# Kernel optimization log

Hardware: AMD Instinct MI355X
Metric: run time of the kernel (lower is better)

The kernel has to match this reference:

```python
import jax, jax.numpy as jnp
import numpy as np

B, S, DIM = 32, 1, 2048
N_HEADS, N_KV = 32, 8
HEAD_DIM = DIM // N_HEADS  # 64
MAXB, MAXS = 32, 2048
START_POS = 2047
THETA = 10000.0  # precompute_freqs_cis called without theta -> llama default


def setup_inputs() -> dict:
    key = jax.random.key(0)
    ks = jax.random.split(key, 7)
    u = lambda k, s: jax.random.uniform(k, s, jnp.float32) * 0.02  # scaled torch.rand init
    return {
        "x": jax.random.normal(ks[0], (B, S, DIM), jnp.float32),
        "q_w": u(ks[1], (DIM, N_HEADS * HEAD_DIM)),
        "k_w": u(ks[2], (DIM, N_KV * HEAD_DIM)),
        "v_w": u(ks[3], (DIM, N_KV * HEAD_DIM)),
        "o_w": u(ks[4], (DIM, N_HEADS * HEAD_DIM)),
        "cache_k": jax.random.normal(ks[5], (MAXB, MAXS, N_KV, HEAD_DIM), jnp.float32) * 0.02,
        "cache_v": jax.random.normal(ks[6], (MAXB, MAXS, N_KV, HEAD_DIM), jnp.float32) * 0.02,
        "start_pos": START_POS,
    }


def _rope(x, cos, sin):
    # x: [B, S, H, D]; consecutive pairs (even, odd) form complex numbers (llama view_as_complex)
    xr, xi = x[..., 0::2], x[..., 1::2]
    out = jnp.stack([xr * cos - xi * sin, xr * sin + xi * cos], axis=-1)
    return out.reshape(x.shape)


def _attn_fwd(x, q_w, k_w, v_w, o_w, cache_k, cache_v, start_pos):
    B_, S_, _ = x.shape
    # fused_linear(x, W) == x @ W
    xq = (x @ q_w).reshape(B_, S_, N_HEADS, HEAD_DIM)
    xk = (x @ k_w).reshape(B_, S_, N_KV, HEAD_DIM)
    xv = (x @ v_w).reshape(B_, S_, N_KV, HEAD_DIM)

    # RoPE freqs for positions [start_pos, start_pos + S)
    inv = 1.0 / (THETA ** (jnp.arange(0, HEAD_DIM, 2, dtype=jnp.float32) / HEAD_DIM))
    t = jnp.arange(start_pos, start_pos + S_, dtype=jnp.float32)
    ang = t[:, None] * inv[None, :]                    # [S, D/2]
    cos = jnp.cos(ang)[None, :, None, :]               # [1, S, 1, D/2]
    sin = jnp.sin(ang)[None, :, None, :]
    xq = _rope(xq, cos, sin)
    xk = _rope(xk, cos, sin)

    # KV-cache append
    cache_k = jax.lax.dynamic_update_slice(cache_k, xk, (0, start_pos, 0, 0))
    cache_v = jax.lax.dynamic_update_slice(cache_v, xv, (0, start_pos, 0, 0))
    L = start_pos + S_
    keys = cache_k[:B_, :L].transpose(0, 2, 1, 3)      # [B, Hkv, L, D]
    vals = cache_v[:B_, :L].transpose(0, 2, 1, 3)

    # GQA attention; grouped einsum = repeat_kv without materializing copies
    rep = N_HEADS // N_KV
    q = xq.transpose(0, 2, 1, 3).reshape(B_, N_KV, rep, S_, HEAD_DIM)
    scores = jnp.einsum('bkrsd,bkld->bkrsl', q, keys) * (HEAD_DIM ** -0.5)
    p = jax.nn.softmax(scores, axis=-1)
    o = jnp.einsum('bkrsl,bkld->bkrsd', p, vals)
    o = o.reshape(B_, N_HEADS, S_, HEAD_DIM).transpose(0, 2, 1, 3).reshape(B_, S_, -1)
    return o @ o_w


def reference(x, q_w, k_w, v_w, o_w, cache_k, cache_v, start_pos):
    return _attn_fwd(x, q_w, k_w, v_w, o_w, cache_k, cache_v, start_pos)
```

## Files before the change

### kernel.cpp

```cpp
#include <hip/hip_runtime.h>
#include <hip/hip_bf16.h>
#include <math.h>

#define NQKV 3072
#define NS 16
#define SPL 128
#define KT 128

__device__ __forceinline__ int read_sp(const int* spp) {
  if (!spp) return 2047;
  int raw = spp[0];
  if (raw >= 0 && raw < 2048) return raw;
  union { int i; float f; } u; u.i = raw;
  if (u.f >= 0.f && u.f < 2048.f) return (int)u.f;
  return 2047;
}

__global__ __launch_bounds__(256) void k_prep(const float* __restrict__ x,
                                              float* __restrict__ xt,
                                              float* __restrict__ rope,
                                              const int* __restrict__ spp) {
  int idx = blockIdx.x * 256 + threadIdx.x;
  int r = idx >> 11, k = idx & 2047;
  xt[k * 32 + r] = x[idx];
  if (blockIdx.x == 0 && threadIdx.x < 32) {
    int i = threadIdx.x;
    int sp = read_sp(spp);
    double freq = pow(10000.0, -(double)(2 * i) / 64.0);
    double ang = (double)sp * freq;
    double sd, cd; sincos(ang, &sd, &cd);
    rope[2 * i]     = (float)cd;
    rope[2 * i + 1] = (float)sd;
  }
}

__global__ __launch_bounds__(256) void k_qkv3(const float* __restrict__ qw,
                                              const float* __restrict__ kw,
                                              const float* __restrict__ vw,
                                              const float* __restrict__ xt,
                                              float* __restrict__ part, int kc) {
  int colb = blockIdx.x, j = blockIdx.y, t = threadIdx.x;
  const float* w; int ldw, col, outcol;
  if (colb < 4)       { w = qw; ldw = 2048; col = colb * 512 + t * 2; outcol = col; }
  else if (colb == 4) { w = kw; ldw = 512;  col = t * 2; outcol = 2048 + col; }
  else                { w = vw; ldw = 512;  col = t * 2; outcol = 2560 + col; }
  __shared__ __align__(16) float xs[KT][32];
  int k0 = j * kc;
  float2 acc[32];
  #pragma unroll
  for (int r = 0; r < 32; r++) { acc[r].x = 0.f; acc[r].y = 0.f; }
  for (int kt = 0; kt < kc; kt += KT) {
    int ksz = (kc - kt < KT) ? (kc - kt) : KT;
    __syncthreads();
    for (int idx = t; idx < ksz * 32; idx += 256)
      ((float*)xs)[idx] = xt[(size_t)(k0 + kt) * 32 + idx];
    __syncthreads();
    const float* wp = w + (size_t)(k0 + kt) * ldw + col;
    #pragma unroll 2
    for (int kk = 0; kk < ksz; kk++) {
      float2 wv = *(const float2*)&wp[(size_t)kk * ldw];
      #pragma unroll
      for (int r4 = 0; r4 < 8; r4++) {
        float4 xr = *(const float4*)&xs[kk][r4 * 4];
        acc[r4*4+0].x = fmaf(xr.x, wv.x, acc[r4*4+0].x);
        acc[r4*4+0].y = fmaf(xr.x, wv.y, acc[r4*4+0].y);
        acc[r4*4+1].x = fmaf(xr.y, wv.x, acc[r4*4+1].x);
        acc[r4*4+1].y = fmaf(xr.y, wv.y, acc[r4*4+1].y);
        acc[r4*4+2].x = fmaf(xr.z, wv.x, acc[r4*4+2].x);
        acc[r4*4+2].y = fmaf(xr.z, wv.y, acc[r4*4+2].y);
        acc[r4*4+3].x = fmaf(xr.w, wv.x, acc[r4*4+3].x);
        acc[r4*4+3].y = fmaf(xr.w, wv.y, acc[r4*4+3].y);
      }
    }
  }
  float* po = part + (size_t)j * (32 * NQKV) + outcol;
  #pragma unroll
  for (int r = 0; r < 32; r++) *(float2*)&po[(size_t)r * NQKV] = acc[r];
}

__global__ __launch_bounds__(256) void k_qred(const float* __restrict__ part,
                                              float* __restrict__ qred, int js) {
  int col = blockIdx.x * 256 + threadIdx.x;
  int b = blockIdx.y;
  float s = 0.f;
  for (int j = 0; j < js; j++) s += part[(size_t)j * (32 * NQKV) + (size_t)b * NQKV + col];
  qred[(size_t)b * NQKV + col] = s;
}

__global__ __launch_bounds__(512) void k_attn3(const float* __restrict__ ck,
                                               const float* __restrict__ cv,
                                               const float* __restrict__ qred,
                                               const float* __restrict__ rope,
                                               float* __restrict__ osplit,
                                               float* __restrict__ msl,
                                               const int* __restrict__ spp) {
  int s = blockIdx.x, b = blockIdx.y, tid = threadIdx.x;
  int sp = read_sp(spp);

  __shared__ __align__(16) float qs[8][4][64];
  __shared__ __align__(16) float knew[8][64];
  __shared__ __align__(16) float vnew[8][64];
  __shared__ __align__(16) float sc[8][4][SPL + 4];
  __shared__ __align__(16) float opart[4][8][4][64];

  const float* qb = qred + (size_t)b * NQKV;

  {
    int pi = tid * 2;
    #pragma unroll
    for (int u = 0; u < 2; u++, pi++) {
      int hq = pi >> 5, i = pi & 31;
      float cs = rope[2 * i], sn = rope[2 * i + 1];
      float a = qb[hq * 64 + 2 * i], bb = qb[hq * 64 + 2 * i + 1];
      qs[hq >> 2][hq & 3][2 * i]     = (a * cs - bb * sn) * 0.125f;
      qs[hq >> 2][hq & 3][2 * i + 1] = (a * sn + bb * cs) * 0.125f;
    }
    if (tid < 256) {
      int h = tid >> 5, i = tid & 31;
      float cs = rope[2 * i], sn = rope[2 * i + 1];
      float a = qb[2048 + h * 64 + 2 * i], bb = qb[2048 + h * 64 + 2 * i + 1];
      knew[h][2 * i]     = a * cs - bb * sn;
      knew[h][2 * i + 1] = a * sn + bb * cs;
    }
    { int h = tid >> 6, d = tid & 63; vnew[h][d] = qb[2560 + h * 64 + d]; }
  }
  __syncthreads();

  int w = tid >> 6, lane = tid & 63;
  int w2 = w >> 1, half = w & 1;
  int hh2 = lane >> 4, d4 = lane & 15;
  int h = half * 4 + hh2;

  float4 qv0 = *(const float4*)&qs[h][0][d4 * 4];
  float4 qv1 = *(const float4*)&qs[h][1][d4 * 4];
  float4 qv2 = *(const float4*)&qs[h][2][d4 * 4];
  float4 qv3 = *(const float4*)&qs[h][3][d4 * 4];
  float4 kn4 = *(const float4*)&knew[h][d4 * 4];
  float4 vn4 = *(const float4*)&vnew[h][d4 * 4];

  const float* kb = ck + (size_t)b * 2048 * 512 + half * 256 + lane * 4;
  int pbase = s * SPL + w2;
  #pragma unroll 4
  for (int i = 0; i < 32; i++) {
    int p = pbase + i * 4;
    float4 k4 = *(const float4*)(kb + (size_t)p * 512);
    if (p == sp) k4 = kn4;
    float s0 = qv0.x * k4.x + qv0.y * k4.y + qv0.z * k4.z + qv0.w * k4.w;
    float s1 = qv1.x * k4.x + qv1.y * k4.y + qv1.z * k4.z + qv1.w * k4.w;
    float s2 = qv2.x * k4.x + qv2.y * k4.y + qv2.z * k4.z + qv2.w * k4.w;
    float s3 = qv3.x * k4.x + qv3.y * k4.y + qv3.z * k4.z + qv3.w * k4.w;
    #pragma unroll
    for (int off = 1; off <= 8; off <<= 1) {
      s0 += __shfl_xor(s0, off);
      s1 += __shfl_xor(s1, off);
      s2 += __shfl_xor(s2, off);
      s3 += __shfl_xor(s3, off);
    }
    float sv = (d4 == 0) ? s0 : (d4 == 1) ? s1 : (d4 == 2) ? s2 : s3;
    if (d4 < 4) sc[h][d4][p - s * SPL] = sv;
  }
  __syncthreads();

  #pragma unroll
  for (int q = 0; q < 4; q++) {
    int row = w * 4 + q, rh = row >> 2, rr = row & 3;
    float2 v01 = *(const float2*)&sc[rh][rr][lane * 2];
    float m = fmaxf(v01.x, v01.y);
    #pragma unroll
    for (int off = 1; off <= 32; off <<= 1) m = fmaxf(m, __shfl_xor(m, off));
    float e0 = __expf(v01.x - m), e1 = __expf(v01.y - m);
    sc[rh][rr][lane * 2] = e0; sc[rh][rr][lane * 2 + 1] = e1;
    float l = e0 + e1;
    #pragma unroll
    for (int off = 1; off <= 32; off <<= 1) l += __shfl_xor(l, off);
    if (lane == 0) {
      size_t mi = (((size_t)b * NS + s) * 32 + row) * 2;
      msl[mi] = m; msl[mi + 1] = l;
    }
  }
  __syncthreads();

  const float* vb = cv + (size_t)b * 2048 * 512 + half * 256 + lane * 4;
  float4 a0 = {0,0,0,0}, a1 = {0,0,0,0}, a2 = {0,0,0,0}, a3 = {0,0,0,0};
  #pragma unroll 4
  for (int i = 0; i < 32; i++) {
    int p = pbase + i * 4;
    float4 v4 = *(const float4*)(vb + (size_t)p * 512);
    if (p == sp) v4 = vn4;
    int pl = p - s * SPL;
    float e0 = sc[h][0][pl], e1 = sc[h][1][pl], e2 = sc[h][2][pl], e3 = sc[h][3][pl];
    a0.x = fmaf(e0, v4.x, a0.x); a0.y = fmaf(e0, v4.y, a0.y);
    a0.z = fmaf(e0, v4.z, a0.z); a0.w = fmaf(e0, v4.w, a0.w);
    a1.x = fmaf(e1, v4.x, a1.x); a1.y = fmaf(e1, v4.y, a1.y);
    a1.z = fmaf(e1, v4.z, a1.z); a1.w = fmaf(e1, v4.w, a1.w);
    a2.x = fmaf(e2, v4.x, a2.x); a2.y = fmaf(e2, v4.y, a2.y);
    a2.z = fmaf(e2, v4.z, a2.z); a2.w = fmaf(e2, v4.w, a2.w);
    a3.x = fmaf(e3, v4.x, a3.x); a3.y = fmaf(e3, v4.y, a3.y);
    a3.z = fmaf(e3, v4.z, a3.z); a3.w = fmaf(e3, v4.w, a3.w);
  }
  *(float4*)&opart[w2][h][0][d4 * 4] = a0;
  *(float4*)&opart[w2][h][1][d4 * 4] = a1;
  *(float4*)&opart[w2][h][2][d4 * 4] = a2;
  *(float4*)&opart[w2][h][3][d4 * 4] = a3;
  __syncthreads();

  for (int e = tid; e < 2048; e += 512) {
    int eh = e >> 8, er = (e >> 6) & 3, ed = e & 63;
    float o = opart[0][eh][er][ed] + opart[1][eh][er][ed] +
              opart[2][eh][er][ed] + opart[3][eh][er][ed];
    osplit[(((size_t)b * NS + s) * 32 + eh * 4 + er) * 64 + ed] = o;
  }
}

__global__ __launch_bounds__(256) void k_combine3(const float* __restrict__ osplit,
                                                  const float* __restrict__ msl,
                                                  float* __restrict__ obt) {
  int b = blockIdx.x, g = blockIdx.y, t = threadIdx.x;
  int hq = g * 8 + (t >> 5);
  int d0 = (t & 31) * 2;
  float ms[NS], ls[NS];
  float m = -1e30f;
  #pragma unroll
  for (int s = 0; s < NS; s++) {
    size_t mi = (((size_t)b * NS + s) * 32 + hq) * 2;
    ms[s] = msl[mi]; ls[s] = msl[mi + 1];
    m = fmaxf(m, ms[s]);
  }
  float L = 0.f, o0 = 0.f, o1 = 0.f;
  #pragma unroll
  for (int s = 0; s < NS; s++) {
    float wgt = __expf(ms[s] - m);
    L = fmaf(wgt, ls[s], L);
    const float* op = osplit + (((size_t)b * NS + s) * 32 + hq) * 64 + d0;
    o0 = fmaf(wgt, op[0], o0);
    o1 = fmaf(wgt, op[1], o1);
  }
  float invL = 1.f / L;
  obt[(size_t)(hq * 64 + d0) * 32 + b]     = o0 * invL;
  obt[(size_t)(hq * 64 + d0 + 1) * 32 + b] = o1 * invL;
}

__global__ __launch_bounds__(256) void k_oproj3(const float* __restrict__ ow,
                                                const float* __restrict__ obt,
                                                float* __restrict__ part, int kc) {
  int colb = blockIdx.x, j = blockIdx.y, t = threadIdx.x;
  int col = colb * 512 + t * 2;
  __shared__ __align__(16) float xs[KT][32];
  int k0 = j * kc;
  float2 acc[32];
  #pragma unroll
  for (int r = 0; r < 32; r++) { acc[r].x = 0.f; acc[r].y = 0.f; }
  for (int kt = 0; kt < kc; kt += KT) {
    int ksz = (kc - kt < KT) ? (kc - kt) : KT;
    __syncthreads();
    for (int idx = t; idx < ksz * 32; idx += 256)
      ((float*)xs)[idx] = obt[(size_t)(k0 + kt) * 32 + idx];
    __syncthreads();
    const float* wp = ow + (size_t)(k0 + kt) * 2048 + col;
    #pragma unroll 2
    for (int kk = 0; kk < ksz; kk++) {
      float2 wv = *(const float2*)&wp[(size_t)kk * 2048];
      #pragma unroll
      for (int r4 = 0; r4 < 8; r4++) {
        float4 xr = *(const float4*)&xs[kk][r4 * 4];
        acc[r4*4+0].x = fmaf(xr.x, wv.x, acc[r4*4+0].x);
        acc[r4*4+0].y = fmaf(xr.x, wv.y, acc[r4*4+0].y);
        acc[r4*4+1].x = fmaf(xr.y, wv.x, acc[r4*4+1].x);
        acc[r4*4+1].y = fmaf(xr.y, wv.y, acc[r4*4+1].y);
        acc[r4*4+2].x = fmaf(xr.z, wv.x, acc[r4*4+2].x);
        acc[r4*4+2].y = fmaf(xr.z, wv.y, acc[r4*4+2].y);
        acc[r4*4+3].x = fmaf(xr.w, wv.x, acc[r4*4+3].x);
        acc[r4*4+3].y = fmaf(xr.w, wv.y, acc[r4*4+3].y);
      }
    }
  }
  float* po = part + (size_t)j * 65536 + col;
  #pragma unroll
  for (int r = 0; r < 32; r++) *(float2*)&po[(size_t)r * 2048] = acc[r];
}

__global__ __launch_bounds__(256) void k_finish(const float* __restrict__ part,
                                                float* __restrict__ out, int js) {
  int idx = blockIdx.x * 256 + threadIdx.x;
  float s = 0.f;
  for (int j = 0; j < js; j++) s += part[(size_t)j * 65536 + idx];
  out[idx] = s;
}

extern "C" void kernel_launch(void* const* d_in, const int* in_sizes, int n_in,
                              void* d_out, int out_size, void* d_ws, size_t ws_size,
                              hipStream_t stream) {
  const float* x  = (const float*)d_in[0];
  const float* qw = (const float*)d_in[1];
  const float* kw = (const float*)d_in[2];
  const float* vw = (const float*)d_in[3];
  const float* ow = (const float*)d_in[4];
  const float* ck = (const float*)d_in[5];
  const float* cv = (const float*)d_in[6];
  const int*   sp = (n_in >= 8) ? (const int*)d_in[7] : nullptr;

  const size_t FIXED = 65536 + 65536 + 98304 + 1048576 + 32768 + 64;
  int js = 2;
  {
    const int cands[5] = {32, 16, 8, 4, 2};
    for (int i = 0; i < 5; i++) {
      if ((FIXED + (size_t)cands[i] * 98304) * 4 <= ws_size) { js = cands[i]; break; }
    }
  }
  int kc = 2048 / js;

  float* ws     = (float*)d_ws;
  float* xt     = ws;
  float* part   = xt + 65536;
  float* obt    = part + (size_t)js * 98304;
  float* qred   = obt + 65536;
  float* osplit = qred + 98304;
  float* msl    = osplit + 1048576;
  float* rope   = msl + 32768;

  k_prep    <<<256,             256, 0, stream>>>(x, xt, rope, sp);
  k_qkv3    <<<dim3(6, js),     256, 0, stream>>>(qw, kw, vw, xt, part, kc);
  k_qred    <<<dim3(12, 32),    256, 0, stream>>>(part, qred, js);
  k_attn3   <<<dim3(NS, 32),    512, 0, stream>>>(ck, cv, qred, rope, osplit, msl, sp);
  k_combine3<<<dim3(32, 4),     256, 0, stream>>>(osplit, msl, obt);
  k_oproj3  <<<dim3(4, js),     256, 0, stream>>>(ow, obt, part, kc);
  k_finish  <<<256,             256, 0, stream>>>(part, (float*)d_out, js);
}
```

Baseline: 418.1 us.

## Fuse split-K reductions via atomics and use single-pass online-softmax attention

The QKV and output projections now accumulate split-K partials with atomicAdd into buffers zeroed in the prep kernel, which removes the separate reduce and finish kernels. The attention kernel switches to a single streaming pass with online softmax, reading K and V together instead of staging scores in shared memory, and each wave now covers 64 contiguous positions. Partial outputs are stored in fp16 across 32 splits per batch, and the combine step merges them. This trades two kernel launches and extra buffer traffic for atomic contention, nondeterministic summation order, and reduced precision in the intermediate attention outputs.

```diff
diff --git a/kernel.cpp b/kernel.cpp
--- a/kernel.cpp
+++ b/kernel.cpp
@@ -1,11 +1,13 @@
 #include <hip/hip_runtime.h>
+#include <hip/hip_fp16.h>
 #include <hip/hip_bf16.h>
 #include <math.h>
 
 #define NQKV 3072
-#define NS 16
-#define SPL 128
-#define KT 128
+#define NS   8
+#define SPL  256
+#define PW   64
+#define NS4  32
 
 __device__ __forceinline__ int read_sp(const int* spp) {
   if (!spp) return 2047;
@@ -16,13 +18,17 @@
   return 2047;
 }
 
-__global__ __launch_bounds__(256) void k_prep(const float* __restrict__ x,
-                                              float* __restrict__ xt,
-                                              float* __restrict__ rope,
-                                              const int* __restrict__ spp) {
+__global__ __launch_bounds__(256) void k_prep5(const float* __restrict__ x,
+                                               float* __restrict__ xt,
+                                               float* __restrict__ qkvacc,
+                                               float* __restrict__ out,
+                                               float* __restrict__ rope,
+                                               const int* __restrict__ spp) {
   int idx = blockIdx.x * 256 + threadIdx.x;
   int r = idx >> 11, k = idx & 2047;
   xt[k * 32 + r] = x[idx];
+  out[idx] = 0.f;
+  for (int z = idx; z < 32 * NQKV; z += 65536) qkvacc[z] = 0.f;
   if (blockIdx.x == 0 && threadIdx.x < 32) {
     int i = threadIdx.x;
     int sp = read_sp(spp);
@@ -34,76 +40,63 @@
   }
 }
 
-__global__ __launch_bounds__(256) void k_qkv3(const float* __restrict__ qw,
+__global__ __launch_bounds__(256) void k_qkv5(const float* __restrict__ qw,
                                               const float* __restrict__ kw,
                                               const float* __restrict__ vw,
                                               const float* __restrict__ xt,
-                                              float* __restrict__ part, int kc) {
+                                              float* __restrict__ qkvacc) {
   int colb = blockIdx.x, j = blockIdx.y, t = threadIdx.x;
   const float* w; int ldw, col, outcol;
   if (colb < 4)       { w = qw; ldw = 2048; col = colb * 512 + t * 2; outcol = col; }
   else if (colb == 4) { w = kw; ldw = 512;  col = t * 2; outcol = 2048 + col; }
   else                { w = vw; ldw = 512;  col = t * 2; outcol = 2560 + col; }
-  __shared__ __align__(16) float xs[KT][32];
-  int k0 = j * kc;
+  __shared__ __align__(16) float xs[64][32];
+  int k0 = j * 64;
+  for (int i2 = t; i2 < 64 * 32; i2 += 256)
+    ((float*)xs)[i2] = xt[(size_t)k0 * 32 + i2];
+  __syncthreads();
   float2 acc[32];
   #pragma unroll
   for (int r = 0; r < 32; r++) { acc[r].x = 0.f; acc[r].y = 0.f; }
-  for (int kt = 0; kt < kc; kt += KT) {
-    int ksz = (kc - kt < KT) ? (kc - kt) : KT;
-    __syncthreads();
-    for (int idx = t; idx < ksz * 32; idx += 256)
-      ((float*)xs)[idx] = xt[(size_t)(k0 + kt) * 32 + idx];
-    __syncthreads();
-    const float* wp = w + (size_t)(k0 + kt) * ldw + col;
-    #pragma unroll 2
-    for (int kk = 0; kk < ksz; kk++) {
-      float2 wv = *(const float2*)&wp[(size_t)kk * ldw];
-      #pragma unroll
-      for (int r4 = 0; r4 < 8; r4++) {
-        float4 xr = *(const float4*)&xs[kk][r4 * 4];
-        acc[r4*4+0].x = fmaf(xr.x, wv.x, acc[r4*4+0].x);
-        acc[r4*4+0].y = fmaf(xr.x, wv.y, acc[r4*4+0].y);
-        acc[r4*4+1].x = fmaf(xr.y, wv.x, acc[r4*4+1].x);
-        acc[r4*4+1].y = fmaf(xr.y, wv.y, acc[r4*4+1].y);
-        acc[r4*4+2].x = fmaf(xr.z, wv.x, acc[r4*4+2].x);
-        acc[r4*4+2].y = fmaf(xr.z, wv.y, acc[r4*4+2].y);
-        acc[r4*4+3].x = fmaf(xr.w, wv.x, acc[r4*4+3].x);
-        acc[r4*4+3].y = fmaf(xr.w, wv.y, acc[r4*4+3].y);
-      }
-    }
-  }
-  float* po = part + (size_t)j * (32 * NQKV) + outcol;
-  #pragma unroll
-  for (int r = 0; r < 32; r++) *(float2*)&po[(size_t)r * NQKV] = acc[r];
-}
-
-__global__ __launch_bounds__(256) void k_qred(const float* __restrict__ part,
-                                              float* __restrict__ qred, int js) {
-  int col = blockIdx.x * 256 + threadIdx.x;
-  int b = blockIdx.y;
-  float s = 0.f;
-  for (int j = 0; j < js; j++) s += part[(size_t)j * (32 * NQKV) + (size_t)b * NQKV + col];
-  qred[(size_t)b * NQKV + col] = s;
-}
-
-__global__ __launch_bounds__(512) void k_attn3(const float* __restrict__ ck,
-                                               const float* __restrict__ cv,
-                                               const float* __restrict__ qred,
-                                               const float* __restrict__ rope,
-                                               float* __restrict__ osplit,
-                                               float* __restrict__ msl,
-                                               const int* __restrict__ spp) {
+  const float* wp = w + (size_t)k0 * ldw + col;
+  #pragma unroll 4
+  for (int kk = 0; kk < 64; kk++) {
+    float2 wv = *(const float2*)&wp[(size_t)kk * ldw];
+    #pragma unroll
+    for (int r4 = 0; r4 < 8; r4++) {
+      float4 xr = *(const float4*)&xs[kk][r4 * 4];
+      acc[r4*4+0].x = fmaf(xr.x, wv.x, acc[r4*4+0].x);
+      acc[r4*4+0].y = fmaf(xr.x, wv.y, acc[r4*4+0].y);
+      acc[r4*4+1].x = fmaf(xr.y, wv.x, acc[r4*4+1].x);
+      acc[r4*4+1].y = fmaf(xr.y, wv.y, acc[r4*4+1].y);
+      acc[r4*4+2].x = fmaf(xr.z, wv.x, acc[r4*4+2].x);
+      acc[r4*4+2].y = fmaf(xr.z, wv.y, acc[r4*4+2].y);
+      acc[r4*4+3].x = fmaf(xr.w, wv.x, acc[r4*4+3].x);
+      acc[r4*4+3].y = fmaf(xr.w, wv.y, acc[r4*4+3].y);
+    }
+  }
+  #pragma unroll
+  for (int r = 0; r < 32; r++) {
+    atomicAdd(&qkvacc[(size_t)r * NQKV + outcol],     acc[r].x);
+    atomicAdd(&qkvacc[(size_t)r * NQKV + outcol + 1], acc[r].y);
+  }
+}
+
+__global__ __launch_bounds__(512, 4) void k_attn5(const float* __restrict__ ck,
+                                                  const float* __restrict__ cv,
+                                                  const float* __restrict__ qkvacc,
+                                                  const float* __restrict__ rope,
+                                                  __half* __restrict__ osplit,
+                                                  float* __restrict__ msl,
+                                                  const int* __restrict__ spp) {
   int s = blockIdx.x, b = blockIdx.y, tid = threadIdx.x;
   int sp = read_sp(spp);
 
   __shared__ __align__(16) float qs[8][4][64];
   __shared__ __align__(16) float knew[8][64];
   __shared__ __align__(16) float vnew[8][64];
-  __shared__ __align__(16) float sc[8][4][SPL + 4];
-  __shared__ __align__(16) float opart[4][8][4][64];
-
-  const float* qb = qred + (size_t)b * NQKV;
+
+  const float* qb = qkvacc + (size_t)b * NQKV;
 
   {
     int pi = tid * 2;
@@ -139,12 +132,19 @@
   float4 vn4 = *(const float4*)&vnew[h][d4 * 4];
 
   const float* kb = ck + (size_t)b * 2048 * 512 + half * 256 + lane * 4;
-  int pbase = s * SPL + w2;
+  const float* vb = cv + (size_t)b * 2048 * 512 + half * 256 + lane * 4;
+  int p0 = s * SPL + w2 * PW;
+
+  float m0 = -1e30f, m1 = -1e30f, m2 = -1e30f, m3 = -1e30f;
+  float l0 = 0.f, l1 = 0.f, l2 = 0.f, l3 = 0.f;
+  float4 o0 = {0,0,0,0}, o1 = {0,0,0,0}, o2 = {0,0,0,0}, o3 = {0,0,0,0};
+
   #pragma unroll 4
-  for (int i = 0; i < 32; i++) {
-    int p = pbase + i * 4;
+  for (int i = 0; i < PW; i++) {
+    int p = p0 + i;
     float4 k4 = *(const float4*)(kb + (size_t)p * 512);
-    if (p == sp) k4 = kn4;
+    float4 v4 = *(const float4*)(vb + (size_t)p * 512);
+    if (p == sp) { k4 = kn4; v4 = vn4; }
     float s0 = qv0.x * k4.x + qv0.y * k4.y + qv0.z * k4.z + qv0.w * k4.w;
     float s1 = qv1.x * k4.x + qv1.y * k4.y + qv1.z * k4.z + qv1.w * k4.w;
     float s2 = qv2.x * k4.x + qv2.y * k4.y + qv2.z * k4.z + qv2.w * k4.w;
@@ -156,135 +156,107 @@
       s2 += __shfl_xor(s2, off);
       s3 += __shfl_xor(s3, off);
     }
-    float sv = (d4 == 0) ? s0 : (d4 == 1) ? s1 : (d4 == 2) ? s2 : s3;
-    if (d4 < 4) sc[h][d4][p - s * SPL] = sv;
-  }
-  __syncthreads();
-
-  #pragma unroll
-  for (int q = 0; q < 4; q++) {
-    int row = w * 4 + q, rh = row >> 2, rr = row & 3;
-    float2 v01 = *(const float2*)&sc[rh][rr][lane * 2];
-    float m = fmaxf(v01.x, v01.y);
-    #pragma unroll
-    for (int off = 1; off <= 32; off <<= 1) m = fmaxf(m, __shfl_xor(m, off));
-    float e0 = __expf(v01.x - m), e1 = __expf(v01.y - m);
-    sc[rh][rr][lane * 2] = e0; sc[rh][rr][lane * 2 + 1] = e1;
-    float l = e0 + e1;
-    #pragma unroll
-    for (int off = 1; off <= 32; off <<= 1) l += __shfl_xor(l, off);
-    if (lane == 0) {
-      size_t mi = (((size_t)b * NS + s) * 32 + row) * 2;
-      msl[mi] = m; msl[mi + 1] = l;
-    }
-  }
-  __syncthreads();
-
-  const float* vb = cv + (size_t)b * 2048 * 512 + half * 256 + lane * 4;
-  float4 a0 = {0,0,0,0}, a1 = {0,0,0,0}, a2 = {0,0,0,0}, a3 = {0,0,0,0};
-  #pragma unroll 4
-  for (int i = 0; i < 32; i++) {
-    int p = pbase + i * 4;
-    float4 v4 = *(const float4*)(vb + (size_t)p * 512);
-    if (p == sp) v4 = vn4;
-    int pl = p - s * SPL;
-    float e0 = sc[h][0][pl], e1 = sc[h][1][pl], e2 = sc[h][2][pl], e3 = sc[h][3][pl];
-    a0.x = fmaf(e0, v4.x, a0.x); a0.y = fmaf(e0, v4.y, a0.y);
-    a0.z = fmaf(e0, v4.z, a0.z); a0.w = fmaf(e0, v4.w, a0.w);
-    a1.x = fmaf(e1, v4.x, a1.x); a1.y = fmaf(e1, v4.y, a1.y);
-    a1.z = fmaf(e1, v4.z, a1.z); a1.w = fmaf(e1, v4.w, a1.w);
-    a2.x = fmaf(e2, v4.x, a2.x); a2.y = fmaf(e2, v4.y, a2.y);
-    a2.z = fmaf(e2, v4.z, a2.z); a2.w = fmaf(e2, v4.w, a2.w);
-    a3.x = fmaf(e3, v4.x, a3.x); a3.y = fmaf(e3, v4.y, a3.y);
-    a3.z = fmaf(e3, v4.z, a3.z); a3.w = fmaf(e3, v4.w, a3.w);
-  }
-  *(float4*)&opart[w2][h][0][d4 * 4] = a0;
-  *(float4*)&opart[w2][h][1][d4 * 4] = a1;
-  *(float4*)&opart[w2][h][2][d4 * 4] = a2;
-  *(float4*)&opart[w2][h][3][d4 * 4] = a3;
-  __syncthreads();
-
-  for (int e = tid; e < 2048; e += 512) {
-    int eh = e >> 8, er = (e >> 6) & 3, ed = e & 63;
-    float o = opart[0][eh][er][ed] + opart[1][eh][er][ed] +
-              opart[2][eh][er][ed] + opart[3][eh][er][ed];
-    osplit[(((size_t)b * NS + s) * 32 + eh * 4 + er) * 64 + ed] = o;
-  }
-}
-
-__global__ __launch_bounds__(256) void k_combine3(const float* __restrict__ osplit,
+    float mn0 = fmaxf(m0, s0), c0 = __expf(m0 - mn0), e0 = __expf(s0 - mn0);
+    float mn1 = fmaxf(m1, s1), c1 = __expf(m1 - mn1), e1 = __expf(s1 - mn1);
+    float mn2 = fmaxf(m2, s2), c2 = __expf(m2 - mn2), e2 = __expf(s2 - mn2);
+    float mn3 = fmaxf(m3, s3), c3 = __expf(m3 - mn3), e3 = __expf(s3 - mn3);
+    l0 = fmaf(l0, c0, e0); l1 = fmaf(l1, c1, e1);
+    l2 = fmaf(l2, c2, e2); l3 = fmaf(l3, c3, e3);
+    m0 = mn0; m1 = mn1; m2 = mn2; m3 = mn3;
+    o0.x = fmaf(e0, v4.x, o0.x * c0); o0.y = fmaf(e0, v4.y, o0.y * c0);
+    o0.z = fmaf(e0, v4.z, o0.z * c0); o0.w = fmaf(e0, v4.w, o0.w * c0);
+    o1.x = fmaf(e1, v4.x, o1.x * c1); o1.y = fmaf(e1, v4.y, o1.y * c1);
+    o1.z = fmaf(e1, v4.z, o1.z * c1); o1.w = fmaf(e1, v4.w, o1.w * c1);
+    o2.x = fmaf(e2, v4.x, o2.x * c2); o2.y = fmaf(e2, v4.y, o2.y * c2);
+    o2.z = fmaf(e2, v4.z, o2.z * c2); o2.w = fmaf(e2, v4.w, o2.w * c2);
+    o3.x = fmaf(e3, v4.x, o3.x * c3); o3.y = fmaf(e3, v4.y, o3.y * c3);
+    o3.z = fmaf(e3, v4.z, o3.z * c3); o3.w = fmaf(e3, v4.w, o3.w * c3);
+  }
+
+  int s4 = s * 4 + w2;
+  size_t rowbase = ((size_t)b * NS4 + s4) * 32;
+  if (d4 == 0) {
+    size_t mi;
+    mi = (rowbase + h * 4 + 0) * 2; msl[mi] = m0; msl[mi + 1] = l0;
+    mi = (rowbase + h * 4 + 1) * 2; msl[mi] = m1; msl[mi + 1] = l1;
+    mi = (rowbase + h * 4 + 2) * 2; msl[mi] = m2; msl[mi + 1] = l2;
+    mi = (rowbase + h * 4 + 3) * 2; msl[mi] = m3; msl[mi + 1] = l3;
+  }
+  {
+    __half* op;
+    op = osplit + (rowbase + h * 4 + 0) * 64 + d4 * 4;
+    op[0] = __float2half(o0.x); op[1] = __float2half(o0.y);
+    op[2] = __float2half(o0.z); op[3] = __float2half(o0.w);
+    op = osplit + (rowbase + h * 4 + 1) * 64 + d4 * 4;
+    op[0] = __float2half(o1.x); op[1] = __float2half(o1.y);
+    op[2] = __float2half(o1.z); op[3] = __float2half(o1.w);
+    op = osplit + (rowbase + h * 4 + 2) * 64 + d4 * 4;
+    op[0] = __float2half(o2.x); op[1] = __float2half(o2.y);
+    op[2] = __float2half(o2.z); op[3] = __float2half(o2.w);
+    op = osplit + (rowbase + h * 4 + 3) * 64 + d4 * 4;
+    op[0] = __float2half(o3.x); op[1] = __float2half(o3.y);
+    op[2] = __float2half(o3.z); op[3] = __float2half(o3.w);
+  }
+}
+
+__global__ __launch_bounds__(256) void k_combine5(const __half* __restrict__ osplit,
                                                   const float* __restrict__ msl,
                                                   float* __restrict__ obt) {
   int b = blockIdx.x, g = blockIdx.y, t = threadIdx.x;
   int hq = g * 8 + (t >> 5);
   int d0 = (t & 31) * 2;
-  float ms[NS], ls[NS];
   float m = -1e30f;
-  #pragma unroll
-  for (int s = 0; s < NS; s++) {
-    size_t mi = (((size_t)b * NS + s) * 32 + hq) * 2;
-    ms[s] = msl[mi]; ls[s] = msl[mi + 1];
-    m = fmaxf(m, ms[s]);
-  }
+  for (int s4 = 0; s4 < NS4; s4++)
+    m = fmaxf(m, msl[(((size_t)b * NS4 + s4) * 32 + hq) * 2]);
   float L = 0.f, o0 = 0.f, o1 = 0.f;
-  #pragma unroll
-  for (int s = 0; s < NS; s++) {
-    float wgt = __expf(ms[s] - m);
-    L = fmaf(wgt, ls[s], L);
-    const float* op = osplit + (((size_t)b * NS + s) * 32 + hq) * 64 + d0;
-    o0 = fmaf(wgt, op[0], o0);
-    o1 = fmaf(wgt, op[1], o1);
+  for (int s4 = 0; s4 < NS4; s4++) {
+    size_t mi = (((size_t)b * NS4 + s4) * 32 + hq) * 2;
+    float wgt = __expf(msl[mi] - m);
+    L = fmaf(wgt, msl[mi + 1], L);
+    const __half* op = osplit + (((size_t)b * NS4 + s4) * 32 + hq) * 64 + d0;
+    o0 = fmaf(wgt, __half2float(op[0]), o0);
+    o1 = fmaf(wgt, __half2float(op[1]), o1);
   }
   float invL = 1.f / L;
   obt[(size_t)(hq * 64 + d0) * 32 + b]     = o0 * invL;
   obt[(size_t)(hq * 64 + d0 + 1) * 32 + b] = o1 * invL;
 }
 
-__global__ __launch_bounds__(256) void k_oproj3(const float* __restrict__ ow,
+__global__ __launch_bounds__(256) void k_oproj5(const float* __restrict__ ow,
                                                 const float* __restrict__ obt,
-                                                float* __restrict__ part, int kc) {
+                                                float* __restrict__ out) {
   int colb = blockIdx.x, j = blockIdx.y, t = threadIdx.x;
   int col = colb * 512 + t * 2;
-  __shared__ __align__(16) float xs[KT][32];
-  int k0 = j * kc;
+  __shared__ __align__(16) float xs[64][32];
+  int k0 = j * 64;
+  for (int i2 = t; i2 < 64 * 32; i2 += 256)
+    ((float*)xs)[i2] = obt[(size_t)k0 * 32 + i2];
+  __syncthreads();
   float2 acc[32];
   #pragma unroll
   for (int r = 0; r < 32; r++) { acc[r].x = 0.f; acc[r].y = 0.f; }
-  for (int kt = 0; kt < kc; kt += KT) {
-    int ksz = (kc - kt < KT) ? (kc - kt) : KT;
-    __syncthreads();
-    for (int idx = t; idx < ksz * 32; idx += 256)
-      ((float*)xs)[idx] = obt[(size_t)(k0 + kt) * 32 + idx];
-    __syncthreads();
-    const float* wp = ow + (size_t)(k0 + kt) * 2048 + col;
-    #pragma unroll 2
-    for (int kk = 0; kk < ksz; kk++) {
-      float2 wv = *(const float2*)&wp[(size_t)kk * 2048];
-      #pragma unroll
-      for (int r4 = 0; r4 < 8; r4++) {
-        float4 xr = *(const float4*)&xs[kk][r4 * 4];
-        acc[r4*4+0].x = fmaf(xr.x, wv.x, acc[r4*4+0].x);
-        acc[r4*4+0].y = fmaf(xr.x, wv.y, acc[r4*4+0].y);
-        acc[r4*4+1].x = fmaf(xr.y, wv.x, acc[r4*4+1].x);
-        acc[r4*4+1].y = fmaf(xr.y, wv.y, acc[r4*4+1].y);
-        acc[r4*4+2].x = fmaf(xr.z, wv.x, acc[r4*4+2].x);
-        acc[r4*4+2].y = fmaf(xr.z, wv.y, acc[r4*4+2].y);
-        acc[r4*4+3].x = fmaf(xr.w, wv.x, acc[r4*4+3].x);
-        acc[r4*4+3].y = fmaf(xr.w, wv.y, acc[r4*4+3].y);
-      }
-    }
-  }
-  float* po = part + (size_t)j * 65536 + col;
-  #pragma unroll
-  for (int r = 0; r < 32; r++) *(float2*)&po[(size_t)r * 2048] = acc[r];
-}
-
-__global__ __launch_bounds__(256) void k_finish(const float* __restrict__ part,
-                                                float* __restrict__ out, int js) {
-  int idx = blockIdx.x * 256 + threadIdx.x;
-  float s = 0.f;
-  for (int j = 0; j < js; j++) s += part[(size_t)j * 65536 + idx];
-  out[idx] = s;
+  const float* wp = ow + (size_t)k0 * 2048 + col;
+  #pragma unroll 4
+  for (int kk = 0; kk < 64; kk++) {
+    float2 wv = *(const float2*)&wp[(size_t)kk * 2048];
+    #pragma unroll
+    for (int r4 = 0; r4 < 8; r4++) {
+      float4 xr = *(const float4*)&xs[kk][r4 * 4];
+      acc[r4*4+0].x = fmaf(xr.x, wv.x, acc[r4*4+0].x);
+      acc[r4*4+0].y = fmaf(xr.x, wv.y, acc[r4*4+0].y);
+      acc[r4*4+1].x = fmaf(xr.y, wv.x, acc[r4*4+1].x);
+      acc[r4*4+1].y = fmaf(xr.y, wv.y, acc[r4*4+1].y);
+      acc[r4*4+2].x = fmaf(xr.z, wv.x, acc[r4*4+2].x);
+      acc[r4*4+2].y = fmaf(xr.z, wv.y, acc[r4*4+2].y);
+      acc[r4*4+3].x = fmaf(xr.w, wv.x, acc[r4*4+3].x);
+      acc[r4*4+3].y = fmaf(xr.w, wv.y, acc[r4*4+3].y);
+    }
+  }
+  #pragma unroll
+  for (int r = 0; r < 32; r++) {
+    atomicAdd(&out[(size_t)r * 2048 + col],     acc[r].x);
+    atomicAdd(&out[(size_t)r * 2048 + col + 1], acc[r].y);
+  }
 }
 
 extern "C" void kernel_launch(void* const* d_in, const int* in_sizes, int n_in,
@@ -299,30 +271,18 @@
   const float* cv = (const float*)d_in[6];
   const int*   sp = (n_in >= 8) ? (const int*)d_in[7] : nullptr;
 
-  const size_t FIXED = 65536 + 65536 + 98304 + 1048576 + 32768 + 64;
-  int js = 2;
-  {
-    const int cands[5] = {32, 16, 8, 4, 2};
-    for (int i = 0; i < 5; i++) {
-      if ((FIXED + (size_t)cands[i] * 98304) * 4 <= ws_size) { js = cands[i]; break; }
-    }
-  }
-  int kc = 2048 / js;
-
   float* ws     = (float*)d_ws;
   float* xt     = ws;
-  float* part   = xt + 65536;
-  float* obt    = part + (size_t)js * 98304;
-  float* qred   = obt + 65536;
-  float* osplit = qred + 98304;
-  float* msl    = osplit + 1048576;
-  float* rope   = msl + 32768;
-
-  k_prep    <<<256,             256, 0, stream>>>(x, xt, rope, sp);
-  k_qkv3    <<<dim3(6, js),     256, 0, stream>>>(qw, kw, vw, xt, part, kc);
-  k_qred    <<<dim3(12, 32),    256, 0, stream>>>(part, qred, js);
-  k_attn3   <<<dim3(NS, 32),    512, 0, stream>>>(ck, cv, qred, rope, osplit, msl, sp);
-  k_combine3<<<dim3(32, 4),     256, 0, stream>>>(osplit, msl, obt);
-  k_oproj3  <<<dim3(4, js),     256, 0, stream>>>(ow, obt, part, kc);
-  k_finish  <<<256,             256, 0, stream>>>(part, (float*)d_out, js);
-}
+  float* qkvacc = xt + 65536;
+  float* obt    = qkvacc + 98304;
+  float* msl    = obt + 65536;
+  float* rope   = msl + 65536;
+  __half* osplit = (__half*)(rope + 64);
+  float* out    = (float*)d_out;
+
+  k_prep5   <<<256,          256, 0, stream>>>(x, xt, qkvacc, out, rope, sp);
+  k_qkv5    <<<dim3(6, 32),  256, 0, stream>>>(qw, kw, vw, xt, qkvacc);
+  k_attn5   <<<dim3(NS, 32), 512, 0, stream>>>(ck, cv, qkvacc, rope, osplit, msl, sp);
+  k_combine5<<<dim3(32, 4),  256, 0, stream>>>(osplit, msl, obt);
+  k_oproj5  <<<dim3(4, 32),  256, 0, stream>>>(ow, obt, out);
+}
```

New measurement: 397.5 us. 1.05x faster.
